# Kernel optimization log

Measured on AMD Instinct MI355X. Metric: run time of the kernel, lower is better.

Reference implementation:

```python
import jax, jax.numpy as jnp
import numpy as np

HIDDEN = 2048
NUM_HEADS = 16
HEAD_DIM = HIDDEN // NUM_HEADS
HARMONICS = 64


def _holo_params(key, in_features, out_features, harmonics):
    kb, kp = jax.random.split(key)
    basis = jax.random.normal(kb, (harmonics, in_features), dtype=jnp.float32)
    basis = basis / jnp.linalg.norm(basis, axis=1, keepdims=True)  # F.normalize(p=2, dim=1)
    phase = jax.random.normal(kp, (out_features, harmonics), dtype=jnp.float32) * 0.1
    amp = jnp.ones((out_features, harmonics), dtype=jnp.float32) / np.sqrt(harmonics).astype(np.float32)
    return basis, phase, amp


def setup_inputs() -> dict:
    key = jax.random.key(0)
    ks = jax.random.split(key, 5)
    hidden_states = jax.random.normal(ks[0], (2, 2048, HIDDEN), dtype=jnp.float32)
    inp = {"hidden_states": hidden_states}
    for name, k in zip(("q", "k", "v", "o"), ks[1:]):
        basis, phase, amp = _holo_params(k, HIDDEN, HIDDEN, HARMONICS)
        inp[f"basis_{name}"] = basis
        inp[f"phase_{name}"] = phase
        inp[f"amp_{name}"] = amp
    return inp


def _holo_linear(x, basis, phase, amp):
    # resonance: (B,S,H) = x @ basis^T; modulated-sum == resonance @ (amp*cos(phase))^T
    resonance = jnp.einsum('bsd,hd->bsh', x, basis)
    w = amp * jnp.cos(phase)  # (out, harmonics)
    return jnp.einsum('bsh,oh->bso', resonance, w)


def reference(hidden_states, basis_q, phase_q, amp_q, basis_k, phase_k, amp_k,
              basis_v, phase_v, amp_v, basis_o, phase_o, amp_o):
    bsz, seq_len, _ = hidden_states.shape
    q = _holo_linear(hidden_states, basis_q, phase_q, amp_q)
    k = _holo_linear(hidden_states, basis_k, phase_k, amp_k)
    v = _holo_linear(hidden_states, basis_v, phase_v, amp_v)
    # (B, H, S, Dh)
    q = q.reshape(bsz, seq_len, NUM_HEADS, HEAD_DIM).transpose(0, 2, 1, 3)
    k = k.reshape(bsz, seq_len, NUM_HEADS, HEAD_DIM).transpose(0, 2, 1, 3)
    v = v.reshape(bsz, seq_len, NUM_HEADS, HEAD_DIM).transpose(0, 2, 1, 3)
    scale = 1.0 / np.sqrt(HEAD_DIM).astype(np.float32)
    scores = jnp.einsum('bhqd,bhkd->bhqk', q, k) * scale
    attn = jax.nn.softmax(scores, axis=-1)
    out = jnp.einsum('bhqk,bhkd->bhqd', attn, v)
    out = out.transpose(0, 2, 1, 3).reshape(bsz, seq_len, HIDDEN)
    return _holo_linear(out, basis_o, phase_o, amp_o)
```

## Files before the change

kernel.cpp:

```cpp
#include <hip/hip_runtime.h>
#include <hip/hip_bf16.h>
#include <math.h>

#define HIDDEN 2048
#define HARM   64
#define NHEADS 16
#define HDIM   128
#define SEQ    2048
#define BATCH  2
#define ROWS   (BATCH*SEQ)
#define RN     (ROWS*HARM)
#define PN     ((size_t)ROWS*HIDDEN)

using bf16x8 = __attribute__((ext_vector_type(8))) short;
using f32x16 = __attribute__((ext_vector_type(16))) float;
using u32x2  = __attribute__((ext_vector_type(2))) unsigned;

#if defined(__has_builtin)
#if __has_builtin(__builtin_amdgcn_exp2f)
#define EXP2F(x) __builtin_amdgcn_exp2f(x)
#else
#define EXP2F(x) exp2f(x)
#endif
#else
#define EXP2F(x) exp2f(x)
#endif

#if defined(__has_builtin) && __has_builtin(__builtin_amdgcn_permlane32_swap)
__device__ inline void plane_swap_u(unsigned& a, unsigned& b) {
  u32x2 r = __builtin_amdgcn_permlane32_swap(a, b, false, false);
  a = r[0]; b = r[1];
}
__device__ inline void plane_swap_f(float& a, float& b) {
  union { float f; unsigned u; } ua, ub;
  ua.f = a; ub.f = b;
  u32x2 r = __builtin_amdgcn_permlane32_swap(ua.u, ub.u, false, false);
  ua.u = r[0]; ub.u = r[1];
  a = ua.f; b = ub.f;
}
#else
__device__ inline void plane_swap_u(unsigned& a, unsigned& b) {
  const bool hi = (threadIdx.x & 32) != 0;
  unsigned ax = (unsigned)__shfl_xor((int)a, 32);
  unsigned bx = (unsigned)__shfl_xor((int)b, 32);
  unsigned r0 = hi ? bx : a;
  unsigned r1 = hi ? b : ax;
  a = r0; b = r1;
}
__device__ inline void plane_swap_f(float& a, float& b) {
  const bool hi = (threadIdx.x & 32) != 0;
  float ax = __shfl_xor(a, 32);
  float bx = __shfl_xor(b, 32);
  float r0 = hi ? bx : a;
  float r1 = hi ? b : ax;
  a = r0; b = r1;
}
#endif

__device__ inline void split_bf(float a, ushort& hi, ushort& lo) {
  __hip_bfloat16 h = __float2bfloat16(a);
  float hf = __bfloat162float(h);
  __hip_bfloat16 l = __float2bfloat16(a - hf);
  union { __hip_bfloat16 b; ushort u; } c1, c2;
  c1.b = h; c2.b = l;
  hi = c1.u; lo = c2.u;
}

__global__ __launch_bounds__(256) void prep(
    const float* __restrict__ X,
    const float* __restrict__ pq, const float* __restrict__ aq,
    const float* __restrict__ pk, const float* __restrict__ ak,
    const float* __restrict__ pv, const float* __restrict__ av,
    const float* __restrict__ po, const float* __restrict__ ao,
    const float* __restrict__ bq, const float* __restrict__ bk,
    const float* __restrict__ bv, const float* __restrict__ bo,
    ushort* __restrict__ Xh, ushort* __restrict__ Xl,
    ushort* __restrict__ Wh, ushort* __restrict__ Wl,
    ushort* __restrict__ Bh, ushort* __restrict__ Bl) {
  const int bid = blockIdx.x;
  const int t = threadIdx.x;
  if (bid < 8192) {
    size_t i = ((size_t)bid * 256 + t) * 4;
    float4 v = *(const float4*)&X[i];
    ushort4 h, l;
    split_bf(v.x, h.x, l.x); split_bf(v.y, h.y, l.y);
    split_bf(v.z, h.z, l.z); split_bf(v.w, h.w, l.w);
    *(ushort4*)&Xh[i] = h;
    *(ushort4*)&Xl[i] = l;
  } else if (bid < 10240) {
    int i = (bid - 8192) * 256 + t;
    const int N = HIDDEN * HARM;
    int set = i / N, j = i - set * N;
    const float* p = (set == 0) ? pq : (set == 1) ? pk : (set == 2) ? pv : po;
    const float* a = (set == 0) ? aq : (set == 1) ? ak : (set == 2) ? av : ao;
    float wv = a[j] * cosf(p[j]);
    ushort h, l;
    split_bf(wv, h, l);
    size_t o = (size_t)set * N + j;
    Wh[o] = h; Wl[o] = l;
  } else {
    int idx = bid - 10240;
    int z = idx >> 7, xb = idx & 127;
    const float* S = (z == 0) ? bq : (z == 1) ? bk : (z == 2) ? bv : bo;
    size_t i = ((size_t)xb * 256 + t) * 4;
    float4 v = *(const float4*)&S[i];
    ushort4 h, l;
    split_bf(v.x, h.x, l.x); split_bf(v.y, h.y, l.y);
    split_bf(v.z, h.z, l.z); split_bf(v.w, h.w, l.w);
    size_t o = (size_t)z * HARM * HIDDEN + i;
    *(ushort4*)&Bh[o] = h;
    *(ushort4*)&Bl[o] = l;
  }
}

__global__ __launch_bounds__(768) void gemm_res3(
    const ushort* __restrict__ Xh, const ushort* __restrict__ Xl,
    const ushort* __restrict__ Bh, const ushort* __restrict__ Bl,
    float* __restrict__ R0, float* __restrict__ R1, float* __restrict__ R2) {
  const int row0 = blockIdx.x * 64;
  const int kc = blockIdx.y;
  __shared__ __align__(16) ushort Xs[2][64][72];
  __shared__ __align__(16) ushort Bs[3][2][64][72];
  const int t = threadIdx.x;
  const int lane = t & 63, w = t >> 6;
  const int l31 = lane & 31, hh = lane >> 5;
  const int z = w >> 2;
  const int wq = w & 3;
  const int m0 = (wq & 1) * 32, n0 = (wq >> 1) * 32;
  f32x16 acc;
  #pragma unroll
  for (int j = 0; j < 16; ++j) acc[j] = 0.0f;

  const int kbase = kc * 512;
  for (int k0 = kbase; k0 < kbase + 512; k0 += 64) {
    #pragma unroll
    for (int it = 0; it < 6; ++it) {
      int idx = t + it * 768;
      if (idx < 4096) {
        int s = idx >> 9, r = (idx >> 3) & 63, c8 = (idx & 7) * 8;
        if (s < 2) {
          const ushort* src = s ? Xl : Xh;
          *(uint4*)&Xs[s][r][c8] =
              *(const uint4*)&src[(size_t)(row0 + r) * HIDDEN + k0 + c8];
        } else {
          int zz = (s - 2) >> 1, pl = (s - 2) & 1;
          const ushort* src = pl ? Bl : Bh;
          *(uint4*)&Bs[zz][pl][r][c8] =
              *(const uint4*)&src[(size_t)zz * HARM * HIDDEN +
                                  (size_t)r * HIDDEN + k0 + c8];
        }
      }
    }
    __syncthreads();
    #pragma unroll
    for (int ks = 0; ks < 4; ++ks) {
      bf16x8 ah = *(const bf16x8*)&Xs[0][m0 + l31][ks * 16 + 8 * hh];
      bf16x8 al = *(const bf16x8*)&Xs[1][m0 + l31][ks * 16 + 8 * hh];
      bf16x8 bh = *(const bf16x8*)&Bs[z][0][n0 + l31][ks * 16 + 8 * hh];
      bf16x8 bl = *(const bf16x8*)&Bs[z][1][n0 + l31][ks * 16 + 8 * hh];
      acc = __builtin_amdgcn_mfma_f32_32x32x16_bf16(ah, bh, acc, 0, 0, 0);
      acc = __builtin_amdgcn_mfma_f32_32x32x16_bf16(al, bh, acc, 0, 0, 0);
      acc = __builtin_amdgcn_mfma_f32_32x32x16_bf16(ah, bl, acc, 0, 0, 0);
    }
    __syncthreads();
  }
  float* Rp = (z == 0) ? R0 : (z == 1) ? R1 : R2;
  float* out = Rp + (size_t)kc * ROWS * HARM;
  #pragma unroll
  for (int r = 0; r < 16; ++r) {
    int mloc = (r & 3) + 8 * (r >> 2) + 4 * hh;
    out[(size_t)(row0 + m0 + mloc) * HARM + n0 + l31] = acc[r];
  }
}

__global__ __launch_bounds__(256) void gemm_res(
    const ushort* __restrict__ Xh, const ushort* __restrict__ Xl,
    const ushort* __restrict__ Bh, const ushort* __restrict__ Bl,
    float* __restrict__ R0, float* __restrict__ R1, float* __restrict__ R2) {
  const int z = blockIdx.z;
  const ushort* Bhz = Bh + (size_t)z * HARM * HIDDEN;
  const ushort* Blz = Bl + (size_t)z * HARM * HIDDEN;
  float* Rp = (z == 0) ? R0 : (z == 1) ? R1 : R2;
  const int row0 = blockIdx.x * 64;
  const int kc = blockIdx.y;
  __shared__ __align__(16) ushort Xs[2][64][72];
  __shared__ __align__(16) ushort Bs[2][64][72];
  const int t = threadIdx.x;
  const int lane = t & 63, w = t >> 6;
  const int l31 = lane & 31, hh = lane >> 5;
  const int m0 = (w & 1) * 32, n0 = (w >> 1) * 32;
  const int srow = t >> 2;
  const int sc = (t & 3) * 16;
  f32x16 acc;
  #pragma unroll
  for (int j = 0; j < 16; ++j) acc[j] = 0.0f;

  const int kbase = kc * 512;
  for (int k0 = kbase; k0 < kbase + 512; k0 += 64) {
    const size_t xo = (size_t)(row0 + srow) * HIDDEN + k0 + sc;
    const size_t bo = (size_t)srow * HIDDEN + k0 + sc;
    *(uint4*)&Xs[0][srow][sc]     = *(const uint4*)&Xh[xo];
    *(uint4*)&Xs[0][srow][sc + 8] = *(const uint4*)&Xh[xo + 8];
    *(uint4*)&Xs[1][srow][sc]     = *(const uint4*)&Xl[xo];
    *(uint4*)&Xs[1][srow][sc + 8] = *(const uint4*)&Xl[xo + 8];
    *(uint4*)&Bs[0][srow][sc]     = *(const uint4*)&Bhz[bo];
    *(uint4*)&Bs[0][srow][sc + 8] = *(const uint4*)&Bhz[bo + 8];
    *(uint4*)&Bs[1][srow][sc]     = *(const uint4*)&Blz[bo];
    *(uint4*)&Bs[1][srow][sc + 8] = *(const uint4*)&Blz[bo + 8];
    __syncthreads();
    #pragma unroll
    for (int ks = 0; ks < 4; ++ks) {
      bf16x8 ah = *(const bf16x8*)&Xs[0][m0 + l31][ks * 16 + 8 * hh];
      bf16x8 al = *(const bf16x8*)&Xs[1][m0 + l31][ks * 16 + 8 * hh];
      bf16x8 bh = *(const bf16x8*)&Bs[0][n0 + l31][ks * 16 + 8 * hh];
      bf16x8 bl = *(const bf16x8*)&Bs[1][n0 + l31][ks * 16 + 8 * hh];
      acc = __builtin_amdgcn_mfma_f32_32x32x16_bf16(ah, bh, acc, 0, 0, 0);
      acc = __builtin_amdgcn_mfma_f32_32x32x16_bf16(al, bh, acc, 0, 0, 0);
      acc = __builtin_amdgcn_mfma_f32_32x32x16_bf16(ah, bl, acc, 0, 0, 0);
    }
    __syncthreads();
  }
  float* out = Rp + (size_t)kc * ROWS * HARM;
  #pragma unroll
  for (int r = 0; r < 16; ++r) {
    int mloc = (r & 3) + 8 * (r >> 2) + 4 * hh;
    out[(size_t)(row0 + m0 + mloc) * HARM + n0 + l31] = acc[r];
  }
}

__global__ __launch_bounds__(256) void gemm_proj(
    const float* __restrict__ Rp0, const float* __restrict__ Rp1,
    const float* __restrict__ Rp2,
    const ushort* __restrict__ Wh, const ushort* __restrict__ Wl,
    ushort* __restrict__ P0, ushort* __restrict__ P1, ushort* __restrict__ Vt) {
  const int z = blockIdx.z;
  const float* Rp = (z == 0) ? Rp0 : (z == 1) ? Rp1 : Rp2;
  const ushort* Whz = Wh + (size_t)z * HIDDEN * HARM;
  const ushort* Wlz = Wl + (size_t)z * HIDDEN * HARM;
  const int row0 = blockIdx.x * 32;
  const int col0 = blockIdx.y * 128;
  __shared__ __align__(16) union PSM {
    struct { ushort Rs[2][32][72]; ushort Ws[2][128][72]; } s;
    ushort ct[128][36];
  } sm;
  const int t = threadIdx.x;
  const int lane = t & 63, w = t >> 6;
  const int l31 = lane & 31, hh = lane >> 5;
  {
    const int r = t >> 3, h0 = (t & 7) * 8;
    const size_t o = (size_t)(row0 + r) * HARM + h0;
    #pragma unroll
    for (int e = 0; e < 8; ++e) {
      float v = Rp[o + e] + Rp[RN + o + e] + Rp[2 * (size_t)RN + o + e] +
                Rp[3 * (size_t)RN + o + e];
      ushort hi, lo;
      split_bf(v, hi, lo);
      sm.s.Rs[0][r][h0 + e] = hi;
      sm.s.Rs[1][r][h0 + e] = lo;
    }
  }
  #pragma unroll
  for (int i = 0; i < 4; ++i) {
    int idx = t + i * 256;
    int o = idx >> 3, c8 = (idx & 7) * 8;
    const size_t go = (size_t)(col0 + o) * HARM + c8;
    *(uint4*)&sm.s.Ws[0][o][c8] = *(const uint4*)&Whz[go];
    *(uint4*)&sm.s.Ws[1][o][c8] = *(const uint4*)&Wlz[go];
  }
  __syncthreads();
  const int n0 = w * 32;
  f32x16 acc;
  #pragma unroll
  for (int j = 0; j < 16; ++j) acc[j] = 0.0f;
  #pragma unroll
  for (int ks = 0; ks < 4; ++ks) {
    bf16x8 ah = *(const bf16x8*)&sm.s.Rs[0][l31][ks * 16 + 8 * hh];
    bf16x8 al = *(const bf16x8*)&sm.s.Rs[1][l31][ks * 16 + 8 * hh];
    bf16x8 bh = *(const bf16x8*)&sm.s.Ws[0][n0 + l31][ks * 16 + 8 * hh];
    bf16x8 bl = *(const bf16x8*)&sm.s.Ws[1][n0 + l31][ks * 16 + 8 * hh];
    acc = __builtin_amdgcn_mfma_f32_32x32x16_bf16(ah, bh, acc, 0, 0, 0);
    acc = __builtin_amdgcn_mfma_f32_32x32x16_bf16(al, bh, acc, 0, 0, 0);
    acc = __builtin_amdgcn_mfma_f32_32x32x16_bf16(ah, bl, acc, 0, 0, 0);
  }
  if (z < 2) {
    ushort* P = (z == 0) ? P0 : P1;
    #pragma unroll
    for (int r = 0; r < 16; ++r) {
      int mloc = (r & 3) + 8 * (r >> 2) + 4 * hh;
      union { __hip_bfloat16 b; ushort u; } cv;
      cv.b = __float2bfloat16(acc[r]);
      P[(size_t)(row0 + mloc) * HIDDEN + col0 + n0 + l31] = cv.u;
    }
  } else {
    __syncthreads();
    #pragma unroll
    for (int r = 0; r < 16; ++r) {
      int mloc = (r & 3) + 8 * (r >> 2) + 4 * hh;
      union { __hip_bfloat16 b; ushort u; } cv;
      cv.b = __float2bfloat16(acc[r]);
      sm.ct[n0 + l31][mloc] = cv.u;
    }
    __syncthreads();
    if (t < 128) {
      const int batch = row0 >> 11;
      const int tok0 = row0 & 2047;
      ushort* dst = Vt + (size_t)batch * SEQ * HIDDEN +
                    (size_t)(col0 + t) * SEQ + tok0;
      #pragma unroll
      for (int j = 0; j < 4; ++j)
        *(uint4*)&dst[j * 8] = *(const uint4*)&sm.ct[t][j * 8];
    }
  }
}

__global__ __launch_bounds__(256) void gemm_proj_f32(
    const float* __restrict__ Rp,
    const ushort* __restrict__ Whz, const ushort* __restrict__ Wlz,
    float* __restrict__ P) {
  const int row0 = blockIdx.x * 32;
  const int col0 = blockIdx.y * 128;
  __shared__ __align__(16) ushort Rs[2][32][72];
  __shared__ __align__(16) ushort Ws[2][128][72];
  const int t = threadIdx.x;
  const int lane = t & 63, w = t >> 6;
  const int l31 = lane & 31, hh = lane >> 5;
  {
    const int r = t >> 3, h0 = (t & 7) * 8;
    const size_t o = (size_t)(row0 + r) * HARM + h0;
    #pragma unroll
    for (int e = 0; e < 8; ++e) {
      float v = Rp[o + e] + Rp[RN + o + e] + Rp[2 * (size_t)RN + o + e] +
                Rp[3 * (size_t)RN + o + e];
      ushort hi, lo;
      split_bf(v, hi, lo);
      Rs[0][r][h0 + e] = hi;
      Rs[1][r][h0 + e] = lo;
    }
  }
  #pragma unroll
  for (int i = 0; i < 4; ++i) {
    int idx = t + i * 256;
    int o = idx >> 3, c8 = (idx & 7) * 8;
    const size_t go = (size_t)(col0 + o) * HARM + c8;
    *(uint4*)&Ws[0][o][c8] = *(const uint4*)&Whz[go];
    *(uint4*)&Ws[1][o][c8] = *(const uint4*)&Wlz[go];
  }
  __syncthreads();
  const int n0 = w * 32;
  f32x16 acc;
  #pragma unroll
  for (int j = 0; j < 16; ++j) acc[j] = 0.0f;
  #pragma unroll
  for (int ks = 0; ks < 4; ++ks) {
    bf16x8 ah = *(const bf16x8*)&Rs[0][l31][ks * 16 + 8 * hh];
    bf16x8 al = *(const bf16x8*)&Rs[1][l31][ks * 16 + 8 * hh];
    bf16x8 bh = *(const bf16x8*)&Ws[0][n0 + l31][ks * 16 + 8 * hh];
    bf16x8 bl = *(const bf16x8*)&Ws[1][n0 + l31][ks * 16 + 8 * hh];
    acc = __builtin_amdgcn_mfma_f32_32x32x16_bf16(ah, bh, acc, 0, 0, 0);
    acc = __builtin_amdgcn_mfma_f32_32x32x16_bf16(al, bh, acc, 0, 0, 0);
    acc = __builtin_amdgcn_mfma_f32_32x32x16_bf16(ah, bl, acc, 0, 0, 0);
  }
  #pragma unroll
  for (int r = 0; r < 16; ++r) {
    int mloc = (r & 3) + 8 * (r >> 2) + 4 * hh;
    P[(size_t)(row0 + mloc) * HIDDEN + col0 + n0 + l31] = acc[r];
  }
}

#define BQ 128
#define BK 64
#define KSTR 136
#define VSTR 72

__device__ inline unsigned pkbf(float a, float b) {
  __hip_bfloat162 h2 = __float22bfloat162_rn(make_float2(a, b));
  union { __hip_bfloat162 h; unsigned u; } cv; cv.h = h2; return cv.u;
}

__global__ __launch_bounds__(256, 2) void attn_mfma(
    const ushort* __restrict__ Qg, const ushort* __restrict__ Kg,
    const ushort* __restrict__ Vt, ushort* __restrict__ Oh,
    ushort* __restrict__ Ol) {
  __shared__ __align__(16) union SM {
    ushort q[BQ][KSTR];
    struct { ushort k[BK][KSTR]; ushort v[HDIM][VSTR]; } kv[2];
  } sm;
  const int t = threadIdx.x;
  const int bh = blockIdx.x & 31;
  const int qt = blockIdx.x >> 5;
  const int b = bh >> 4, h = bh & 15;
  const int q0 = qt * BQ;
  const int lane = t & 63;
  const int w = t >> 6;
  const int l31 = lane & 31;
  const int hh = lane >> 5;
  const float SC2 = 0.08838834764831845f * 1.4426950408889634f;

  const int sk_key = t >> 4;
  const int sk_d0 = (t & 15) * 8;
  const int sv_d = t >> 3;
  const int sv_k = (t & 7) * 8;
  const size_t kbase = ((size_t)(b * SEQ)) * HIDDEN + h * HDIM;
  const size_t vbase = ((size_t)(b * SEQ + h * HDIM)) * SEQ;

  {
    const size_t gbase = ((size_t)(b * SEQ + q0)) * HIDDEN + h * HDIM;
    for (int p = 0; p < 8; ++p) {
      int row = p * 16 + sk_key;
      uint4 v = *(const uint4*)&Qg[gbase + (size_t)row * HIDDEN + sk_d0];
      *(uint4*)&sm.q[row][sk_d0] = v;
    }
  }
  __syncthreads();
  bf16x8 Qf[8];
  {
    const int qrow = w * 32 + l31;
    #pragma unroll
    for (int ks = 0; ks < 8; ++ks)
      Qf[ks] = *(const bf16x8*)&sm.q[qrow][ks * 16 + 8 * hh];
  }
  __syncthreads();

  float mrow = -1e30f, lsum = 0.0f;
  f32x16 Ot[4];
  #pragma unroll
  for (int i = 0; i < 4; ++i)
    #pragma unroll
    for (int j = 0; j < 16; ++j) Ot[i][j] = 0.0f;
  f32x16 Zv;
  #pragma unroll
  for (int j = 0; j < 16; ++j) Zv[j] = 0.0f;

  uint4 kp[4], vp[4];
  {
    const size_t gb = kbase;
    #pragma unroll
    for (int p = 0; p < 4; ++p)
      kp[p] = *(const uint4*)&Kg[gb + (size_t)(p * 16 + sk_key) * HIDDEN + sk_d0];
    #pragma unroll
    for (int p = 0; p < 4; ++p)
      vp[p] = *(const uint4*)&Vt[vbase + (size_t)(p * 32 + sv_d) * SEQ + sv_k];
    #pragma unroll
    for (int p = 0; p < 4; ++p)
      *(uint4*)&sm.kv[0].k[p * 16 + sk_key][sk_d0] = kp[p];
    #pragma unroll
    for (int p = 0; p < 4; ++p)
      *(uint4*)&sm.kv[0].v[p * 32 + sv_d][sv_k] = vp[p];
  }
  __syncthreads();

  for (int ci = 0; ci < 32; ++ci) {
    {
      const int cn = (ci < 31) ? ci + 1 : 31;
      const size_t gb = kbase + (size_t)(cn * BK) * HIDDEN;
      #pragma unroll
      for (int p = 0; p < 4; ++p)
        kp[p] = *(const uint4*)&Kg[gb + (size_t)(p * 16 + sk_key) * HIDDEN + sk_d0];
      const size_t vb = vbase + cn * BK;
      #pragma unroll
      for (int p = 0; p < 4; ++p)
        vp[p] = *(const uint4*)&Vt[vb + (size_t)(p * 32 + sv_d) * SEQ + sv_k];
    }
    const int cb = ci & 1;

    f32x16 C0, C1;
    {
      bf16x8 a0 = *(const bf16x8*)&sm.kv[cb].k[l31][8 * hh];
      bf16x8 a1 = *(const bf16x8*)&sm.kv[cb].k[32 + l31][8 * hh];
      __builtin_amdgcn_s_setprio(1);
      C0 = __builtin_amdgcn_mfma_f32_32x32x16_bf16(a0, Qf[0], Zv, 0, 0, 0);
      C1 = __builtin_amdgcn_mfma_f32_32x32x16_bf16(a1, Qf[0], Zv, 0, 0, 0);
      #pragma unroll
      for (int ks = 1; ks < 8; ++ks) {
        bf16x8 b0 = *(const bf16x8*)&sm.kv[cb].k[l31][ks * 16 + 8 * hh];
        bf16x8 b1 = *(const bf16x8*)&sm.kv[cb].k[32 + l31][ks * 16 + 8 * hh];
        C0 = __builtin_amdgcn_mfma_f32_32x32x16_bf16(b0, Qf[ks], C0, 0, 0, 0);
        C1 = __builtin_amdgcn_mfma_f32_32x32x16_bf16(b1, Qf[ks], C1, 0, 0, 0);
      }
      __builtin_amdgcn_s_setprio(0);
    }

    float m01[16];
    #pragma unroll
    for (int j = 0; j < 16; ++j) m01[j] = fmaxf(C0[j], C1[j]);
    float x0 = fmaxf(fmaxf(m01[0], m01[1]), m01[2]);
    float x1 = fmaxf(fmaxf(m01[3], m01[4]), m01[5]);
    float x2 = fmaxf(fmaxf(m01[6], m01[7]), m01[8]);
    float x3 = fmaxf(fmaxf(m01[9], m01[10]), m01[11]);
    float x4 = fmaxf(fmaxf(m01[12], m01[13]), m01[14]);
    float mxr = fmaxf(fmaxf(fmaxf(x0, x1), fmaxf(x2, x3)), fmaxf(x4, m01[15]));
    {
      float u = mxr, v2 = mxr;
      plane_swap_f(u, v2);
      mxr = fmaxf(u, v2);
    }

    const float mg = mxr * SC2;
    if (__any(mg > mrow)) {
      const float mnew = fmaxf(mrow, mg);
      const float alpha = EXP2F(mrow - mnew);
      lsum *= alpha;
      #pragma unroll
      for (int i = 0; i < 4; ++i)
        #pragma unroll
        for (int j = 0; j < 16; ++j) Ot[i][j] *= alpha;
      mrow = mnew;
    }
    float s0 = 0.0f, s1 = 0.0f, s2 = 0.0f, s3 = 0.0f;
    #pragma unroll
    for (int j = 0; j < 16; ++j) {
      float e0 = EXP2F(fmaf(C0[j], SC2, -mrow));
      float e1 = EXP2F(fmaf(C1[j], SC2, -mrow));
      C0[j] = e0; C1[j] = e1;
      if (j & 1) { s2 += e0; s3 += e1; } else { s0 += e0; s1 += e1; }
    }
    lsum += (s0 + s1) + (s2 + s3);

    #pragma unroll
    for (int st = 0; st < 4; ++st) {
      const int eb = 8 * (st & 1);
      unsigned A0, A1, B0, B1;
      if (st < 2) {
        A0 = pkbf(C0[eb + 0], C0[eb + 1]); A1 = pkbf(C0[eb + 2], C0[eb + 3]);
        B0 = pkbf(C0[eb + 4], C0[eb + 5]); B1 = pkbf(C0[eb + 6], C0[eb + 7]);
      } else {
        A0 = pkbf(C1[eb + 0], C1[eb + 1]); A1 = pkbf(C1[eb + 2], C1[eb + 3]);
        B0 = pkbf(C1[eb + 4], C1[eb + 5]); B1 = pkbf(C1[eb + 6], C1[eb + 7]);
      }
      plane_swap_u(A0, B0);
      plane_swap_u(A1, B1);
      union { unsigned u[4]; bf16x8 v; } cv;
      cv.u[0] = A0; cv.u[1] = A1; cv.u[2] = B0; cv.u[3] = B1;
      __builtin_amdgcn_s_setprio(1);
      #pragma unroll
      for (int mt = 0; mt < 4; ++mt) {
        bf16x8 a2 = *(const bf16x8*)&sm.kv[cb].v[mt * 32 + l31][st * 16 + 8 * hh];
        Ot[mt] = __builtin_amdgcn_mfma_f32_32x32x16_bf16(a2, cv.v, Ot[mt], 0, 0, 0);
      }
      __builtin_amdgcn_s_setprio(0);
    }

    {
      const int nb = cb ^ 1;
      #pragma unroll
      for (int p = 0; p < 4; ++p)
        *(uint4*)&sm.kv[nb].k[p * 16 + sk_key][sk_d0] = kp[p];
      #pragma unroll
      for (int p = 0; p < 4; ++p)
        *(uint4*)&sm.kv[nb].v[p * 32 + sv_d][sv_k] = vp[p];
    }
    __syncthreads();
  }

  {
    float u = lsum, v2 = lsum;
    plane_swap_f(u, v2);
    lsum = u + v2;
  }
  const float inv = 1.0f / lsum;
  const int qrow = q0 + w * 32 + l31;
  const size_t ob = ((size_t)(b * SEQ + qrow)) * HIDDEN + h * HDIM;
  #pragma unroll
  for (int mt = 0; mt < 4; ++mt)
    #pragma unroll
    for (int g = 0; g < 4; ++g) {
      ushort4 hs, ls;
      split_bf(Ot[mt][4 * g + 0] * inv, hs.x, ls.x);
      split_bf(Ot[mt][4 * g + 1] * inv, hs.y, ls.y);
      split_bf(Ot[mt][4 * g + 2] * inv, hs.z, ls.z);
      split_bf(Ot[mt][4 * g + 3] * inv, hs.w, ls.w);
      const size_t off = ob + mt * 32 + 8 * g + 4 * hh;
      *(ushort4*)&Oh[off] = hs;
      *(ushort4*)&Ol[off] = ls;
    }
}

extern "C" void kernel_launch(void* const* d_in, const int* in_sizes, int n_in,
                              void* d_out, int out_size, void* d_ws, size_t ws_size,
                              hipStream_t stream) {
  (void)in_sizes; (void)n_in; (void)out_size; (void)ws_size;
  const float* X       = (const float*)d_in[0];
  const float* basis_q = (const float*)d_in[1];
  const float* phase_q = (const float*)d_in[2];
  const float* amp_q   = (const float*)d_in[3];
  const float* basis_k = (const float*)d_in[4];
  const float* phase_k = (const float*)d_in[5];
  const float* amp_k   = (const float*)d_in[6];
  const float* basis_v = (const float*)d_in[7];
  const float* phase_v = (const float*)d_in[8];
  const float* amp_v   = (const float*)d_in[9];
  const float* basis_o = (const float*)d_in[10];
  const float* phase_o = (const float*)d_in[11];
  const float* amp_o   = (const float*)d_in[12];

  const size_t WN = (size_t)HIDDEN * HARM;

  char* p = (char*)d_ws;
  ushort* Xhi = (ushort*)p; p += PN * 2;
  ushort* Xlo = (ushort*)p; p += PN * 2;
  ushort* Bhi = (ushort*)p; p += 4 * WN * 2;
  ushort* Blo = (ushort*)p; p += 4 * WN * 2;
  ushort* Whi = (ushort*)p; p += 4 * WN * 2;
  ushort* Wlo = (ushort*)p; p += 4 * WN * 2;
  float* Rqp = (float*)p; p += (size_t)4 * RN * 4;
  float* Rkp = (float*)p; p += (size_t)4 * RN * 4;
  float* Rvp = (float*)p; p += (size_t)4 * RN * 4;
  float* Rop = (float*)p; p += (size_t)4 * RN * 4;
  __hip_bfloat16* Qb = (__hip_bfloat16*)p; p += PN * 2;
  __hip_bfloat16* Kb = (__hip_bfloat16*)p; p += PN * 2;
  __hip_bfloat16* VtB = (__hip_bfloat16*)p; p += PN * 2;
  ushort* AOh = (ushort*)p; p += PN * 2;
  ushort* AOl = (ushort*)p; p += PN * 2;
  float* out = (float*)d_out;

  prep<<<10752, 256, 0, stream>>>(X,
                                  phase_q, amp_q, phase_k, amp_k,
                                  phase_v, amp_v, phase_o, amp_o,
                                  basis_q, basis_k, basis_v, basis_o,
                                  Xhi, Xlo, Whi, Wlo, Bhi, Blo);

  gemm_res3<<<dim3(64, 4), 768, 0, stream>>>(Xhi, Xlo, Bhi, Blo, Rqp, Rkp, Rvp);

  gemm_proj<<<dim3(128, 16, 3), 256, 0, stream>>>(
      Rqp, Rkp, Rvp, Whi, Wlo, (ushort*)Qb, (ushort*)Kb, (ushort*)VtB);

  attn_mfma<<<dim3((SEQ / BQ) * 32), 256, 0, stream>>>(
      (const ushort*)Qb, (const ushort*)Kb, (const ushort*)VtB, AOh, AOl);

  gemm_res<<<dim3(64, 4, 1), 256, 0, stream>>>(
      AOh, AOl, Bhi + 3 * WN, Blo + 3 * WN, Rop, Rop, Rop);

  gemm_proj_f32<<<dim3(128, 16), 256, 0, stream>>>(
      Rop, Whi + 3 * WN, Wlo + 3 * WN, out);
}
```

Measured before the change: 268.8 us.

## Single-buffer attention LDS for higher occupancy and revert fused QKV resonance GEMM

The attention kernel drops the double-buffered K/V shared-memory tiles in favour of a single buffer guarded by an extra barrier, and raises the launch bound to four blocks per CU. The aim is higher occupancy to hide latency, at the cost of an extra sync per chunk and tighter register limits that may cause spills. The fused three-projection resonance GEMM (gemm_res3, 768 threads) is removed and the generic gemm_res kernel is launched over three z-slices instead, which re-reads the X tiles once per projection.

```diff
diff --git a/kernel.cpp b/kernel.cpp
--- a/kernel.cpp
+++ b/kernel.cpp
@@ -113,66 +113,6 @@
   }
 }
 
-__global__ __launch_bounds__(768) void gemm_res3(
-    const ushort* __restrict__ Xh, const ushort* __restrict__ Xl,
-    const ushort* __restrict__ Bh, const ushort* __restrict__ Bl,
-    float* __restrict__ R0, float* __restrict__ R1, float* __restrict__ R2) {
-  const int row0 = blockIdx.x * 64;
-  const int kc = blockIdx.y;
-  __shared__ __align__(16) ushort Xs[2][64][72];
-  __shared__ __align__(16) ushort Bs[3][2][64][72];
-  const int t = threadIdx.x;
-  const int lane = t & 63, w = t >> 6;
-  const int l31 = lane & 31, hh = lane >> 5;
-  const int z = w >> 2;
-  const int wq = w & 3;
-  const int m0 = (wq & 1) * 32, n0 = (wq >> 1) * 32;
-  f32x16 acc;
-  #pragma unroll
-  for (int j = 0; j < 16; ++j) acc[j] = 0.0f;
-
-  const int kbase = kc * 512;
-  for (int k0 = kbase; k0 < kbase + 512; k0 += 64) {
-    #pragma unroll
-    for (int it = 0; it < 6; ++it) {
-      int idx = t + it * 768;
-      if (idx < 4096) {
-        int s = idx >> 9, r = (idx >> 3) & 63, c8 = (idx & 7) * 8;
-        if (s < 2) {
-          const ushort* src = s ? Xl : Xh;
-          *(uint4*)&Xs[s][r][c8] =
-              *(const uint4*)&src[(size_t)(row0 + r) * HIDDEN + k0 + c8];
-        } else {
-          int zz = (s - 2) >> 1, pl = (s - 2) & 1;
-          const ushort* src = pl ? Bl : Bh;
-          *(uint4*)&Bs[zz][pl][r][c8] =
-              *(const uint4*)&src[(size_t)zz * HARM * HIDDEN +
-                                  (size_t)r * HIDDEN + k0 + c8];
-        }
-      }
-    }
-    __syncthreads();
-    #pragma unroll
-    for (int ks = 0; ks < 4; ++ks) {
-      bf16x8 ah = *(const bf16x8*)&Xs[0][m0 + l31][ks * 16 + 8 * hh];
-      bf16x8 al = *(const bf16x8*)&Xs[1][m0 + l31][ks * 16 + 8 * hh];
-      bf16x8 bh = *(const bf16x8*)&Bs[z][0][n0 + l31][ks * 16 + 8 * hh];
-      bf16x8 bl = *(const bf16x8*)&Bs[z][1][n0 + l31][ks * 16 + 8 * hh];
-      acc = __builtin_amdgcn_mfma_f32_32x32x16_bf16(ah, bh, acc, 0, 0, 0);
-      acc = __builtin_amdgcn_mfma_f32_32x32x16_bf16(al, bh, acc, 0, 0, 0);
-      acc = __builtin_amdgcn_mfma_f32_32x32x16_bf16(ah, bl, acc, 0, 0, 0);
-    }
-    __syncthreads();
-  }
-  float* Rp = (z == 0) ? R0 : (z == 1) ? R1 : R2;
-  float* out = Rp + (size_t)kc * ROWS * HARM;
-  #pragma unroll
-  for (int r = 0; r < 16; ++r) {
-    int mloc = (r & 3) + 8 * (r >> 2) + 4 * hh;
-    out[(size_t)(row0 + m0 + mloc) * HARM + n0 + l31] = acc[r];
-  }
-}
-
 __global__ __launch_bounds__(256) void gemm_res(
     const ushort* __restrict__ Xh, const ushort* __restrict__ Xl,
     const ushort* __restrict__ Bh, const ushort* __restrict__ Bl,
@@ -377,13 +317,13 @@
   union { __hip_bfloat162 h; unsigned u; } cv; cv.h = h2; return cv.u;
 }
 
-__global__ __launch_bounds__(256, 2) void attn_mfma(
+__global__ __launch_bounds__(256, 4) void attn_mfma(
     const ushort* __restrict__ Qg, const ushort* __restrict__ Kg,
     const ushort* __restrict__ Vt, ushort* __restrict__ Oh,
     ushort* __restrict__ Ol) {
   __shared__ __align__(16) union SM {
     ushort q[BQ][KSTR];
-    struct { ushort k[BK][KSTR]; ushort v[HDIM][VSTR]; } kv[2];
+    struct { ushort k[BK][KSTR]; ushort v[HDIM][VSTR]; } kv;
   } sm;
   const int t = threadIdx.x;
   const int bh = blockIdx.x & 31;
@@ -442,10 +382,10 @@
       vp[p] = *(const uint4*)&Vt[vbase + (size_t)(p * 32 + sv_d) * SEQ + sv_k];
     #pragma unroll
     for (int p = 0; p < 4; ++p)
-      *(uint4*)&sm.kv[0].k[p * 16 + sk_key][sk_d0] = kp[p];
+      *(uint4*)&sm.kv.k[p * 16 + sk_key][sk_d0] = kp[p];
     #pragma unroll
     for (int p = 0; p < 4; ++p)
-      *(uint4*)&sm.kv[0].v[p * 32 + sv_d][sv_k] = vp[p];
+      *(uint4*)&sm.kv.v[p * 32 + sv_d][sv_k] = vp[p];
   }
   __syncthreads();
 
@@ -461,19 +401,18 @@
       for (int p = 0; p < 4; ++p)
         vp[p] = *(const uint4*)&Vt[vb + (size_t)(p * 32 + sv_d) * SEQ + sv_k];
     }
-    const int cb = ci & 1;
 
     f32x16 C0, C1;
     {
-      bf16x8 a0 = *(const bf16x8*)&sm.kv[cb].k[l31][8 * hh];
-      bf16x8 a1 = *(const bf16x8*)&sm.kv[cb].k[32 + l31][8 * hh];
+      bf16x8 a0 = *(const bf16x8*)&sm.kv.k[l31][8 * hh];
+      bf16x8 a1 = *(const bf16x8*)&sm.kv.k[32 + l31][8 * hh];
       __builtin_amdgcn_s_setprio(1);
       C0 = __builtin_amdgcn_mfma_f32_32x32x16_bf16(a0, Qf[0], Zv, 0, 0, 0);
       C1 = __builtin_amdgcn_mfma_f32_32x32x16_bf16(a1, Qf[0], Zv, 0, 0, 0);
       #pragma unroll
       for (int ks = 1; ks < 8; ++ks) {
-        bf16x8 b0 = *(const bf16x8*)&sm.kv[cb].k[l31][ks * 16 + 8 * hh];
-        bf16x8 b1 = *(const bf16x8*)&sm.kv[cb].k[32 + l31][ks * 16 + 8 * hh];
+        bf16x8 b0 = *(const bf16x8*)&sm.kv.k[l31][ks * 16 + 8 * hh];
+        bf16x8 b1 = *(const bf16x8*)&sm.kv.k[32 + l31][ks * 16 + 8 * hh];
         C0 = __builtin_amdgcn_mfma_f32_32x32x16_bf16(b0, Qf[ks], C0, 0, 0, 0);
         C1 = __builtin_amdgcn_mfma_f32_32x32x16_bf16(b1, Qf[ks], C1, 0, 0, 0);
       }
@@ -534,21 +473,19 @@
       __builtin_amdgcn_s_setprio(1);
       #pragma unroll
       for (int mt = 0; mt < 4; ++mt) {
-        bf16x8 a2 = *(const bf16x8*)&sm.kv[cb].v[mt * 32 + l31][st * 16 + 8 * hh];
+        bf16x8 a2 = *(const bf16x8*)&sm.kv.v[mt * 32 + l31][st * 16 + 8 * hh];
         Ot[mt] = __builtin_amdgcn_mfma_f32_32x32x16_bf16(a2, cv.v, Ot[mt], 0, 0, 0);
       }
       __builtin_amdgcn_s_setprio(0);
     }
 
-    {
-      const int nb = cb ^ 1;
-      #pragma unroll
-      for (int p = 0; p < 4; ++p)
-        *(uint4*)&sm.kv[nb].k[p * 16 + sk_key][sk_d0] = kp[p];
-      #pragma unroll
-      for (int p = 0; p < 4; ++p)
-        *(uint4*)&sm.kv[nb].v[p * 32 + sv_d][sv_k] = vp[p];
-    }
+    __syncthreads();
+    #pragma unroll
+    for (int p = 0; p < 4; ++p)
+      *(uint4*)&sm.kv.k[p * 16 + sk_key][sk_d0] = kp[p];
+    #pragma unroll
+    for (int p = 0; p < 4; ++p)
+      *(uint4*)&sm.kv.v[p * 32 + sv_d][sv_k] = vp[p];
     __syncthreads();
   }
 
@@ -619,7 +556,7 @@
                                   basis_q, basis_k, basis_v, basis_o,
                                   Xhi, Xlo, Whi, Wlo, Bhi, Blo);
 
-  gemm_res3<<<dim3(64, 4), 768, 0, stream>>>(Xhi, Xlo, Bhi, Blo, Rqp, Rkp, Rvp);
+  gemm_res<<<dim3(64, 4, 3), 256, 0, stream>>>(Xhi, Xlo, Bhi, Blo, Rqp, Rkp, Rvp);
 
   gemm_proj<<<dim3(128, 16, 3), 256, 0, stream>>>(
       Rqp, Rkp, Rvp, Whi, Wlo, (ushort*)Qb, (ushort*)Kb, (ushort*)VtB);
```

Result: slower. 472.4 us (+75.7%).
